# Kernel tuning notes

Hardware: AMD Instinct MI355X
Metric: run time of the kernel (lower is better)

Reference implementation:

```python
import jax, jax.numpy as jnp
import numpy as np

B, S, I, H, O = 64, 2048, 128, 256, 128


def setup_inputs() -> dict:
    key = jax.random.key(0)
    ks = jax.random.split(key, 7)
    s = 1.0 / np.sqrt(H)
    return {
        "x": jax.random.normal(ks[0], (B, S, I), dtype=jnp.float32),
        "W_ih": jax.random.uniform(ks[1], (H, I), jnp.float32, -s, s),
        "W_hh": jax.random.uniform(ks[2], (H, H), jnp.float32, -s, s),
        "b_ih": jax.random.uniform(ks[3], (H,), jnp.float32, -s, s),
        "b_hh": jax.random.uniform(ks[4], (H,), jnp.float32, -s, s),
        "W_fc": jax.random.uniform(ks[5], (O, H), jnp.float32, -s, s),
        "b_fc": jax.random.uniform(ks[6], (O,), jnp.float32, -s, s),
    }


def reference(x, W_ih, W_hh, b_ih, b_hh, W_fc, b_fc):
    # h_t = tanh(x_t @ W_ih^T + h_{t-1} @ W_hh^T + b_ih + b_hh)
    b = b_ih + b_hh
    # Precompute input projection for all timesteps in one GEMM: [B,S,H]
    xproj = jnp.einsum('bsi,hi->bsh', x, W_ih) + b

    def step(h, xp_t):  # h: [B,H], xp_t: [B,H]
        h_next = jnp.tanh(xp_t + h @ W_hh.T)
        return h_next, h_next

    h0 = jnp.zeros((B, H), dtype=x.dtype)
    _, hs = jax.lax.scan(step, h0, jnp.swapaxes(xproj, 0, 1))  # hs: [S,B,H]
    hidden_states = jnp.swapaxes(hs, 0, 1)  # [B,S,H]
    outputs = jnp.einsum('bsh,oh->bso', hidden_states, W_fc) + b_fc  # [B,S,O]
    return outputs, hidden_states
```

## Files before the change

### kernel.cpp

```cpp
#include <hip/hip_runtime.h>

#define BB 64
#define SS 2048
#define II 128
#define HH 256
#define OO 128

typedef _Float16 h2_t  __attribute__((ext_vector_type(2)));
typedef _Float16 half8 __attribute__((ext_vector_type(8)));
typedef float    f32x4 __attribute__((ext_vector_type(4)));

__device__ __forceinline__ h2_t u2h(unsigned u) {
    union { unsigned u; h2_t h; } c; c.u = u; return c.h;
}

#if __has_builtin(__builtin_amdgcn_fdot2)
__device__ __forceinline__ float fdot2(unsigned h, unsigned w, float acc) {
    return __builtin_amdgcn_fdot2(u2h(h), u2h(w), acc, false);
}
#else
__device__ __forceinline__ float fdot2(unsigned h, unsigned w, float acc) {
    h2_t hh = u2h(h), ww = u2h(w);
    acc = fmaf((float)hh.x, (float)hh.x * 0.f + (float)ww.x, acc);
    acc = fmaf((float)hh.y, (float)ww.y, acc);
    return acc;
}
#endif

__global__ void prep_kernel(const float* __restrict__ W_ih, const float* __restrict__ b_ih,
                            const float* __restrict__ b_hh, const float* __restrict__ W_fc,
                            float* __restrict__ biasc, unsigned* __restrict__ wsw,
                            unsigned* __restrict__ wfcp, unsigned* __restrict__ wihp,
                            const float* __restrict__ W_hh) {
    int idx = blockIdx.x * 256 + threadIdx.x;
    if (idx < HH * (HH / 2)) {
        int d   = idx & 3;
        int s   = idx >> 2;
        int l   = s & 63;
        int rem = s >> 6;
        int i    = rem & 7;
        int pair = (rem >> 3) & 1;
        int w    = rem >> 4;
        int j    = w * 32 + (l & 15) * 2 + pair;
        int word = (l >> 4) * 32 + i * 4 + d;
        union { h2_t h; unsigned u; } pk;
        pk.h.x = (_Float16)W_hh[j * HH + 2 * word];
        pk.h.y = (_Float16)W_hh[j * HH + 2 * word + 1];
        wsw[idx] = pk.u;
    }
    if (idx < 8 * 8 * 64 * 4) {
        int d    = idx & 3;
        int slot = idx >> 2;
        int l    = slot & 63;
        int kt   = (slot >> 6) & 7;
        int jt   = slot >> 9;
        int j    = jt * 16 + (l & 15);
        int k0   = kt * 32 + (l >> 4) * 8 + d * 2;
        union { h2_t h; unsigned u; } pk;
        pk.h.x = (_Float16)W_fc[j * HH + k0];
        pk.h.y = (_Float16)W_fc[j * HH + k0 + 1];
        wfcp[idx] = pk.u;
    }
    if (idx < 16 * 4 * 64 * 4) {
        int d    = idx & 3;
        int slot = idx >> 2;
        int l    = slot & 63;
        int kt   = (slot >> 6) & 3;
        int jt   = slot >> 8;
        int j    = jt * 16 + (l & 15);
        int k0   = kt * 32 + (l >> 4) * 8 + d * 2;
        union { h2_t h; unsigned u; } pk;
        pk.h.x = (_Float16)W_ih[j * II + k0];
        pk.h.y = (_Float16)W_ih[j * II + k0 + 1];
        wihp[idx] = pk.u;
    }
    if (idx < HH) biasc[idx] = b_ih[idx] + b_hh[idx];
}

__global__ __launch_bounds__(256, 4)
void gemm1_mfma(const float* __restrict__ x, const unsigned* __restrict__ wihp,
                const float* __restrict__ biasc, float* __restrict__ xproj) {
    const int tid = threadIdx.x;
    const int w   = tid >> 6;
    const int l   = tid & 63;
    const int krow = l >> 4;
    const long r  = (long)blockIdx.x * 64 + w * 16 + (l & 15);
    const float* __restrict__ xrow = x + r * II;

    f32x4 acc[16];
#pragma unroll
    for (int jt = 0; jt < 16; ++jt) acc[jt] = (f32x4){0.f, 0.f, 0.f, 0.f};

#pragma unroll
    for (int kt = 0; kt < 4; ++kt) {
        float4 h0 = *(const float4*)&xrow[kt * 32 + krow * 8];
        float4 h1 = *(const float4*)&xrow[kt * 32 + krow * 8 + 4];
        half8 bf;
        bf[0] = (_Float16)h0.x; bf[1] = (_Float16)h0.y;
        bf[2] = (_Float16)h0.z; bf[3] = (_Float16)h0.w;
        bf[4] = (_Float16)h1.x; bf[5] = (_Float16)h1.y;
        bf[6] = (_Float16)h1.z; bf[7] = (_Float16)h1.w;
#pragma unroll
        for (int jt = 0; jt < 16; ++jt) {
            half8 af = *(const half8*)&wihp[(size_t)((jt * 4 + kt) * 64 + l) * 4];
            acc[jt] = __builtin_amdgcn_mfma_f32_16x16x32_f16(af, bf, acc[jt], 0, 0, 0);
        }
    }

#pragma unroll
    for (int jt = 0; jt < 16; ++jt) {
        int j0 = jt * 16 + krow * 4;
        float4 bb = *(const float4*)&biasc[j0];
        float4 o;
        o.x = acc[jt][0] + bb.x; o.y = acc[jt][1] + bb.y;
        o.z = acc[jt][2] + bb.z; o.w = acc[jt][3] + bb.w;
        *(float4*)&xproj[r * HH + j0] = o;
    }
}

__global__ __launch_bounds__(256, 4)
void gemm2_mfma(const float* __restrict__ hidden, const unsigned* __restrict__ wfcp,
                const float* __restrict__ b_fc, float* __restrict__ out) {
    const int tid = threadIdx.x;
    const int w   = tid >> 6;
    const int l   = tid & 63;
    const int krow = l >> 4;
    const long r  = (long)blockIdx.x * 64 + w * 16 + (l & 15);
    const float* __restrict__ hrow = hidden + r * HH;

    f32x4 acc[8];
#pragma unroll
    for (int jt = 0; jt < 8; ++jt) acc[jt] = (f32x4){0.f, 0.f, 0.f, 0.f};

#pragma unroll
    for (int kt = 0; kt < 8; ++kt) {
        float4 h0 = *(const float4*)&hrow[kt * 32 + krow * 8];
        float4 h1 = *(const float4*)&hrow[kt * 32 + krow * 8 + 4];
        half8 bf;
        bf[0] = (_Float16)h0.x; bf[1] = (_Float16)h0.y;
        bf[2] = (_Float16)h0.z; bf[3] = (_Float16)h0.w;
        bf[4] = (_Float16)h1.x; bf[5] = (_Float16)h1.y;
        bf[6] = (_Float16)h1.z; bf[7] = (_Float16)h1.w;
#pragma unroll
        for (int jt = 0; jt < 8; ++jt) {
            half8 af = *(const half8*)&wfcp[(size_t)((jt * 8 + kt) * 64 + l) * 4];
            acc[jt] = __builtin_amdgcn_mfma_f32_16x16x32_f16(af, bf, acc[jt], 0, 0, 0);
        }
    }

#pragma unroll
    for (int jt = 0; jt < 8; ++jt) {
        int j0 = jt * 16 + krow * 4;
        float4 bb = *(const float4*)&b_fc[j0];
        float4 o;
        o.x = acc[jt][0] + bb.x; o.y = acc[jt][1] + bb.y;
        o.z = acc[jt][2] + bb.z; o.w = acc[jt][3] + bb.w;
        *(float4*)&out[r * OO + j0] = o;
    }
}

__global__ __attribute__((amdgpu_waves_per_eu(2, 2))) __launch_bounds__(512)
void rnn_scan(const unsigned* __restrict__ wsw, float* __restrict__ hid) {
    const int b   = blockIdx.x;
    const int tid = threadIdx.x;
    const int w   = tid >> 6;
    const int l   = tid & 63;
    const int sl  = l & 15;
    const int q   = l >> 4;

    const int j0 = w * 32 + sl * 2;

    __shared__ __align__(16) unsigned h16[2][4 * 36];

    const uint4* __restrict__ wp = (const uint4*)wsw + ((size_t)w << 10) + l;

    for (int i = tid; i < 2 * 4 * 36; i += 512) ((unsigned*)h16)[i] = 0u;

    float* __restrict__ base = hid + (size_t)b * SS * HH;
    float2 xp0 = *(const float2*)&base[j0];
    float2 xp1 = *(const float2*)&base[HH + j0];
    __syncthreads();

#pragma unroll 1
    for (int t = 0; t < SS; ++t) {
        uint4 wA[8], wB[8];
#pragma unroll
        for (int i = 0; i < 8; ++i) {
            wA[i] = wp[i * 64];
            wB[i] = wp[(8 + i) * 64];
        }

        float2 xp2 = make_float2(0.f, 0.f);
        if (t + 2 < SS) xp2 = *(const float2*)&base[(size_t)(t + 2) * HH + j0];

        const uint4* hb = (const uint4*)&h16[t & 1][q * 36];
        float aA0 = 0.f, aA1 = 0.f, aB0 = 0.f, aB1 = 0.f;
#pragma unroll
        for (int i = 0; i < 8; ++i) {
            uint4 hv = hb[i];
            aA0 = fdot2(hv.x, wA[i].x, aA0);
            aA1 = fdot2(hv.y, wA[i].y, aA1);
            aA0 = fdot2(hv.z, wA[i].z, aA0);
            aA1 = fdot2(hv.w, wA[i].w, aA1);
            aB0 = fdot2(hv.x, wB[i].x, aB0);
            aB1 = fdot2(hv.y, wB[i].y, aB1);
            aB0 = fdot2(hv.z, wB[i].z, aB0);
            aB1 = fdot2(hv.w, wB[i].w, aB1);
        }
        float sA = aA0 + aA1;
        float sB = aB0 + aB1;
        sA += __shfl_xor(sA, 16, 64);
        sA += __shfl_xor(sA, 32, 64);
        sB += __shfl_xor(sB, 16, 64);
        sB += __shfl_xor(sB, 32, 64);

        float s0 = xp0.x + sA;
        float s1 = xp0.y + sB;
        float e0  = __expf(2.0f * s0);
        float e1  = __expf(2.0f * s1);
        float hn0 = 1.0f - __fdividef(2.0f, e0 + 1.0f);
        float hn1 = 1.0f - __fdividef(2.0f, e1 + 1.0f);

        if (q == 0) {
            union { h2_t h; unsigned u; } pk;
            pk.h.x = (_Float16)hn0;
            pk.h.y = (_Float16)hn1;
            const int W = j0 >> 1;
            h16[(t & 1) ^ 1][(W >> 5) * 36 + (W & 31)] = pk.u;
            *(float2*)&base[(size_t)t * HH + j0] = make_float2(hn0, hn1);
        }
        __syncthreads();
        xp0 = xp1;
        xp1 = xp2;
    }
}

extern "C" void kernel_launch(void* const* d_in, const int* in_sizes, int n_in,
                              void* d_out, int out_size, void* d_ws, size_t ws_size,
                              hipStream_t stream) {
    const float* x    = (const float*)d_in[0];
    const float* W_ih = (const float*)d_in[1];
    const float* W_hh = (const float*)d_in[2];
    const float* b_ih = (const float*)d_in[3];
    const float* b_hh = (const float*)d_in[4];
    const float* W_fc = (const float*)d_in[5];
    const float* b_fc = (const float*)d_in[6];

    float* out_fc  = (float*)d_out;
    float* hidden  = (float*)d_out + (size_t)BB * SS * OO;

    float*    biasc = (float*)d_ws;
    unsigned* wsw   = (unsigned*)(biasc + HH);
    unsigned* wfcp  = wsw + HH * (HH / 2);
    unsigned* wihp  = wfcp + 8 * 8 * 64 * 4;

    const long NR = (long)BB * SS;

    prep_kernel<<<128, 256, 0, stream>>>(W_ih, b_ih, b_hh, W_fc,
                                         biasc, wsw, wfcp, wihp, W_hh);
    gemm1_mfma<<<NR / 64, 256, 0, stream>>>(x, wihp, biasc, hidden);
    rnn_scan<<<BB, 512, 0, stream>>>(wsw, hidden);
    gemm2_mfma<<<NR / 64, 256, 0, stream>>>(hidden, wfcp, b_fc, out_fc);
}
```

Baseline: 1.353 ms.

## Switch recurrent scan from fp16 dot2 to fp32 FMA with new weight layout

The recurrent matvec now keeps W_hh and the hidden state in fp32 and uses plain FMAs instead of packed fp16 dot2. Weights are re-swizzled so each lane covers 4 output rows over a 32-wide k slice, with an 8-way k split reduced by a shuffle butterfly. This doubles the weight bytes re-read from cache every step and the FMA count, in exchange for full-precision recurrence and a different reduction pattern. An asm barrier on the weight pointer stops the compiler from hoisting the loads out of the loop.

```diff
diff --git a/kernel.cpp b/kernel.cpp
--- a/kernel.cpp
+++ b/kernel.cpp
@@ -10,43 +10,23 @@
 typedef _Float16 half8 __attribute__((ext_vector_type(8)));
 typedef float    f32x4 __attribute__((ext_vector_type(4)));
 
-__device__ __forceinline__ h2_t u2h(unsigned u) {
-    union { unsigned u; h2_t h; } c; c.u = u; return c.h;
-}
-
-#if __has_builtin(__builtin_amdgcn_fdot2)
-__device__ __forceinline__ float fdot2(unsigned h, unsigned w, float acc) {
-    return __builtin_amdgcn_fdot2(u2h(h), u2h(w), acc, false);
-}
-#else
-__device__ __forceinline__ float fdot2(unsigned h, unsigned w, float acc) {
-    h2_t hh = u2h(h), ww = u2h(w);
-    acc = fmaf((float)hh.x, (float)hh.x * 0.f + (float)ww.x, acc);
-    acc = fmaf((float)hh.y, (float)ww.y, acc);
-    return acc;
-}
-#endif
-
 __global__ void prep_kernel(const float* __restrict__ W_ih, const float* __restrict__ b_ih,
                             const float* __restrict__ b_hh, const float* __restrict__ W_fc,
-                            float* __restrict__ biasc, unsigned* __restrict__ wsw,
+                            float* __restrict__ biasc, float* __restrict__ wswf,
                             unsigned* __restrict__ wfcp, unsigned* __restrict__ wihp,
                             const float* __restrict__ W_hh) {
     int idx = blockIdx.x * 256 + threadIdx.x;
-    if (idx < HH * (HH / 2)) {
-        int d   = idx & 3;
-        int s   = idx >> 2;
-        int l   = s & 63;
+    if (idx < HH * HH) {
+        int d = idx & 3;
+        int s = idx >> 2;
+        int l = s & 63;
         int rem = s >> 6;
-        int i    = rem & 7;
-        int pair = (rem >> 3) & 1;
-        int w    = rem >> 4;
-        int j    = w * 32 + (l & 15) * 2 + pair;
-        int word = (l >> 4) * 32 + i * 4 + d;
-        union { h2_t h; unsigned u; } pk;
-        pk.h.x = (_Float16)W_hh[j * HH + 2 * word];
-        pk.h.y = (_Float16)W_hh[j * HH + 2 * word + 1];
-        wsw[idx] = pk.u;
+        int i = rem & 7;
+        int o = (rem >> 3) & 3;
+        int w = rem >> 5;
+        int j = w * 32 + (l & 7) * 4 + o;
+        int k = (l >> 3) * 32 + i * 4 + d;
+        wswf[idx] = W_hh[j * HH + k];
     }
     if (idx < 8 * 8 * 64 * 4) {
         int d    = idx & 3;
@@ -160,74 +140,88 @@
 }
 
 __global__ __attribute__((amdgpu_waves_per_eu(2, 2))) __launch_bounds__(512)
-void rnn_scan(const unsigned* __restrict__ wsw, float* __restrict__ hid) {
+void rnn_scan(const float* __restrict__ wswf, float* __restrict__ hid) {
     const int b   = blockIdx.x;
     const int tid = threadIdx.x;
     const int w   = tid >> 6;
     const int l   = tid & 63;
-    const int sl  = l & 15;
-    const int q   = l >> 4;
-
-    const int j0 = w * 32 + sl * 2;
-
-    __shared__ __align__(16) unsigned h16[2][4 * 36];
-
-    const uint4* __restrict__ wp = (const uint4*)wsw + ((size_t)w << 10) + l;
-
-    for (int i = tid; i < 2 * 4 * 36; i += 512) ((unsigned*)h16)[i] = 0u;
+    const int sl  = l & 7;
+    const int q   = l >> 3;
+    const int g   = q >> 1;
+
+    const int jown = w * 32 + sl * 4 + g;
+
+    __shared__ __align__(16) float hbuf[2][8 * 36];
+
+    uintptr_t wpa = (uintptr_t)((const float4*)wswf + ((size_t)w << 11) + l);
+
+    for (int i = tid; i < 2 * 8 * 36; i += 512) ((float*)hbuf)[i] = 0.0f;
 
     float* __restrict__ base = hid + (size_t)b * SS * HH;
-    float2 xp0 = *(const float2*)&base[j0];
-    float2 xp1 = *(const float2*)&base[HH + j0];
+    float xp0 = base[jown];
+    float xp1 = base[HH + jown];
     __syncthreads();
 
 #pragma unroll 1
     for (int t = 0; t < SS; ++t) {
-        uint4 wA[8], wB[8];
+        asm volatile("" : "+v"(wpa));
+        const float4* __restrict__ wpm = (const float4*)wpa;
+
+        float4 w0[8], w1[8], w2[8], w3[8];
 #pragma unroll
         for (int i = 0; i < 8; ++i) {
-            wA[i] = wp[i * 64];
-            wB[i] = wp[(8 + i) * 64];
-        }
-
-        float2 xp2 = make_float2(0.f, 0.f);
-        if (t + 2 < SS) xp2 = *(const float2*)&base[(size_t)(t + 2) * HH + j0];
-
-        const uint4* hb = (const uint4*)&h16[t & 1][q * 36];
-        float aA0 = 0.f, aA1 = 0.f, aB0 = 0.f, aB1 = 0.f;
+            w0[i] = wpm[i * 64];
+            w1[i] = wpm[512 + i * 64];
+            w2[i] = wpm[1024 + i * 64];
+            w3[i] = wpm[1536 + i * 64];
+        }
+
+        const int t2 = (t + 2 < SS) ? (t + 2) : (SS - 1);
+        float xp2 = base[(size_t)t2 * HH + jown];
+
+        const float4* hb = (const float4*)&hbuf[t & 1][q * 36];
+        float p0 = 0.f, p1 = 0.f, p2 = 0.f, p3 = 0.f;
 #pragma unroll
         for (int i = 0; i < 8; ++i) {
-            uint4 hv = hb[i];
-            aA0 = fdot2(hv.x, wA[i].x, aA0);
-            aA1 = fdot2(hv.y, wA[i].y, aA1);
-            aA0 = fdot2(hv.z, wA[i].z, aA0);
-            aA1 = fdot2(hv.w, wA[i].w, aA1);
-            aB0 = fdot2(hv.x, wB[i].x, aB0);
-            aB1 = fdot2(hv.y, wB[i].y, aB1);
-            aB0 = fdot2(hv.z, wB[i].z, aB0);
-            aB1 = fdot2(hv.w, wB[i].w, aB1);
-        }
-        float sA = aA0 + aA1;
-        float sB = aB0 + aB1;
-        sA += __shfl_xor(sA, 16, 64);
-        sA += __shfl_xor(sA, 32, 64);
-        sB += __shfl_xor(sB, 16, 64);
-        sB += __shfl_xor(sB, 32, 64);
-
-        float s0 = xp0.x + sA;
-        float s1 = xp0.y + sB;
-        float e0  = __expf(2.0f * s0);
-        float e1  = __expf(2.0f * s1);
-        float hn0 = 1.0f - __fdividef(2.0f, e0 + 1.0f);
-        float hn1 = 1.0f - __fdividef(2.0f, e1 + 1.0f);
-
-        if (q == 0) {
-            union { h2_t h; unsigned u; } pk;
-            pk.h.x = (_Float16)hn0;
-            pk.h.y = (_Float16)hn1;
-            const int W = j0 >> 1;
-            h16[(t & 1) ^ 1][(W >> 5) * 36 + (W & 31)] = pk.u;
-            *(float2*)&base[(size_t)t * HH + j0] = make_float2(hn0, hn1);
+            float4 hv = hb[i];
+            p0 = fmaf(hv.x, w0[i].x, p0);
+            p0 = fmaf(hv.y, w0[i].y, p0);
+            p0 = fmaf(hv.z, w0[i].z, p0);
+            p0 = fmaf(hv.w, w0[i].w, p0);
+            p1 = fmaf(hv.x, w1[i].x, p1);
+            p1 = fmaf(hv.y, w1[i].y, p1);
+            p1 = fmaf(hv.z, w1[i].z, p1);
+            p1 = fmaf(hv.w, w1[i].w, p1);
+            p2 = fmaf(hv.x, w2[i].x, p2);
+            p2 = fmaf(hv.y, w2[i].y, p2);
+            p2 = fmaf(hv.z, w2[i].z, p2);
+            p2 = fmaf(hv.w, w2[i].w, p2);
+            p3 = fmaf(hv.x, w3[i].x, p3);
+            p3 = fmaf(hv.y, w3[i].y, p3);
+            p3 = fmaf(hv.z, w3[i].z, p3);
+            p3 = fmaf(hv.w, w3[i].w, p3);
+        }
+
+        p0 += __shfl_xor(p0, 8, 64);
+        p1 += __shfl_xor(p1, 8, 64);
+        p2 += __shfl_xor(p2, 8, 64);
+        p3 += __shfl_xor(p3, 8, 64);
+
+        float s  = (g == 0) ? p0 : (g == 1) ? p1 : (g == 2) ? p2 : p3;
+        float x1 = (g == 0) ? p1 : (g == 1) ? p0 : (g == 2) ? p3 : p2;
+        s += __shfl_xor(x1, 16, 64);
+        float x2 = (g == 0) ? p2 : (g == 1) ? p3 : (g == 2) ? p0 : p1;
+        s += __shfl_xor(x2, 32, 64);
+        float x3 = (g == 0) ? p3 : (g == 1) ? p2 : (g == 2) ? p1 : p0;
+        s += __shfl_xor(x3, 48, 64);
+
+        s += xp0;
+        float e  = __expf(2.0f * s);
+        float hn = 1.0f - __fdividef(2.0f, e + 1.0f);
+
+        if (!(q & 1)) {
+            hbuf[(t & 1) ^ 1][(jown >> 5) * 36 + (jown & 31)] = hn;
+            base[(size_t)t * HH + jown] = hn;
         }
         __syncthreads();
         xp0 = xp1;
@@ -250,15 +244,15 @@
     float* hidden  = (float*)d_out + (size_t)BB * SS * OO;
 
     float*    biasc = (float*)d_ws;
-    unsigned* wsw   = (unsigned*)(biasc + HH);
-    unsigned* wfcp  = wsw + HH * (HH / 2);
+    float*    wswf  = biasc + HH;
+    unsigned* wfcp  = (unsigned*)(wswf + HH * HH);
     unsigned* wihp  = wfcp + 8 * 8 * 64 * 4;
 
     const long NR = (long)BB * SS;
 
-    prep_kernel<<<128, 256, 0, stream>>>(W_ih, b_ih, b_hh, W_fc,
-                                         biasc, wsw, wfcp, wihp, W_hh);
+    prep_kernel<<<256, 256, 0, stream>>>(W_ih, b_ih, b_hh, W_fc,
+                                         biasc, wswf, wfcp, wihp, W_hh);
     gemm1_mfma<<<NR / 64, 256, 0, stream>>>(x, wihp, biasc, hidden);
-    rnn_scan<<<BB, 512, 0, stream>>>(wsw, hidden);
+    rnn_scan<<<BB, 512, 0, stream>>>(wswf, hidden);
     gemm2_mfma<<<NR / 64, 256, 0, stream>>>(hidden, wfcp, b_fc, out_fc);
 }
```

Measured after the change: 4.983 ms. 268% more time.
